# Kernel tuning notes

Measured on AMD Instinct MI355X. Metric: run time of the kernel, lower is better.

## Reference

```python
import jax, jax.numpy as jnp
import numpy as np

GRID = 12  # sqrt(144), seq_len = 144 fixed by w_g shape


def _relative_position(n: int) -> jnp.ndarray:
    # grid cell centers for an n x n grid, flattened row-major -> (n*n,)
    idx = np.arange(n * n)
    row, col = idx // n, idx % n
    cx = (col + 0.5) / n  # (x_min + x_max)/2 with x_min=col/n, x_max=(col+1)/n
    cy = (row + 0.5) / n
    dx = cx[:, None] - cx[None, :]
    dy = cy[:, None] - cy[None, :]
    ax = np.sign(dx) * 0.5
    ay = np.sign(dy) * 0.5
    dx = np.abs(np.log(np.abs(dx) + 0.5))
    dy = np.abs(np.log(np.abs(dy) + 0.5))
    # cat along leading dim then permute(1,2,0) == stack last-dim in order (dx,dy,ax,ay)
    pos = np.stack([dx, dy, ax, ay], axis=-1).astype(np.float32)  # (S,S,4)
    return jnp.asarray(pos)


def setup_inputs() -> dict:
    key = jax.random.key(0)
    ks = jax.random.split(key, 9)
    B, S, D = 128, GRID * GRID, 1024
    sc = 1.0 / np.sqrt(D)
    return {
        "query": jax.random.normal(ks[0], (B, S, D), jnp.float32),
        "key": jax.random.normal(ks[1], (B, S, D), jnp.float32),
        "value": jax.random.normal(ks[2], (B, S, D), jnp.float32),
        "Wq": jax.random.normal(ks[3], (D, D), jnp.float32) * sc,
        "bq": jnp.zeros((D,), jnp.float32),
        "Wk": jax.random.normal(ks[4], (D, D), jnp.float32) * sc,
        "bk": jnp.zeros((D,), jnp.float32),
        "Wv": jax.random.normal(ks[5], (D, D), jnp.float32) * sc,
        "bv": jnp.zeros((D,), jnp.float32),
        "Wlin": jax.random.normal(ks[6], (D, 4), jnp.float32) * 0.5,
        "w_g": jax.random.normal(ks[7], (S, D, 1), jnp.float32) * sc,
    }


def reference(query, key, value, Wq, bq, Wk, bk, Wv, bv, Wlin, w_g):
    d_model = query.shape[-1]
    # QKV projections + ReLU activation (dropout is identity at eval)
    q = jax.nn.relu(jnp.einsum("bsd,ed->bse", query, Wq) + bq)
    k = jax.nn.relu(jnp.einsum("bsd,ed->bse", key, Wk) + bk)
    v = jax.nn.relu(jnp.einsum("bsd,ed->bse", value, Wv) + bv)
    # raw scores: (B, S, S)
    att = jnp.einsum("bsd,btd->bst", q, k) * (d_model ** -0.5)
    # relative-position bias: (S, S, 4) -> linear -> relu -> per-row w_g -> relu
    pos = _relative_position(GRID)
    rp = jax.nn.relu(jnp.einsum("stf,df->std", pos, Wlin))  # (S, S, D)
    rp = jax.nn.relu(jnp.einsum("std,sdo->sto", rp, w_g)[..., 0])  # (S, S)
    att = jax.nn.softmax(att + rp[None, :, :], axis=-1)
    return jnp.einsum("bst,btd->bsd", att, v)
```

## Files before the change

### kernel.cpp

```cpp
#include <hip/hip_runtime.h>
#include <hip/hip_fp16.h>

#define DEV __device__ __forceinline__

using half8 = __attribute__((ext_vector_type(8))) _Float16;
using half4 = __attribute__((ext_vector_type(4))) _Float16;
using f32x4 = __attribute__((ext_vector_type(4))) float;

DEV void gload_lds16(const void* g, void* l) {
  __builtin_amdgcn_global_load_lds((const __attribute__((address_space(1))) unsigned int*)g,
                                   (__attribute__((address_space(3))) unsigned int*)l,
                                   16, 0, 0);
}

DEV f32x4 mfma16x32(half8 a, half8 b, f32x4 c) {
  return __builtin_amdgcn_mfma_f32_16x16x32_f16(a, b, c, 0, 0, 0);
}

__global__ void conv3_f32_f16(const float* __restrict__ s0, const float* __restrict__ s1,
                              const float* __restrict__ s2, _Float16* __restrict__ d0,
                              _Float16* __restrict__ d1, _Float16* __restrict__ d2, int n) {
  const float* s = blockIdx.z == 0 ? s0 : (blockIdx.z == 1 ? s1 : s2);
  _Float16* d = blockIdx.z == 0 ? d0 : (blockIdx.z == 1 ? d1 : d2);
  int i = (blockIdx.x * 256 + threadIdx.x) * 8;
  if (i >= n) return;
  float4 a = *(const float4*)(s + i);
  float4 b = *(const float4*)(s + i + 4);
  half8 h;
  h[0] = (_Float16)a.x; h[1] = (_Float16)a.y; h[2] = (_Float16)a.z; h[3] = (_Float16)a.w;
  h[4] = (_Float16)b.x; h[5] = (_Float16)b.y; h[6] = (_Float16)b.z; h[7] = (_Float16)b.w;
  *(half8*)(d + i) = h;
}

__global__ __launch_bounds__(192) void rp_kernel(const float* __restrict__ Wlin,
                                                 const float* __restrict__ wg,
                                                 float* __restrict__ rp) {
  int s = blockIdx.x, t = threadIdx.x;
  if (t >= 144) return;
  int rs = s / 12, cs = s % 12, rt = t / 12, ct = t % 12;
  float dx = (cs - ct) / 12.f, dy = (rs - rt) / 12.f;
  float ax = (dx > 0.f) ? 0.5f : (dx < 0.f ? -0.5f : 0.f);
  float ay = (dy > 0.f) ? 0.5f : (dy < 0.f ? -0.5f : 0.f);
  float lx = fabsf(logf(fabsf(dx) + 0.5f));
  float ly = fabsf(logf(fabsf(dy) + 0.5f));
  float a0 = 0.f, a1 = 0.f, a2 = 0.f, a3 = 0.f;
  const float* wgs = wg + s * 1024;
  for (int d = 0; d < 1024; d += 4) {
#pragma unroll
    for (int u = 0; u < 4; ++u) {
      float4 w = *(const float4*)(Wlin + (d + u) * 4);
      float dot = lx * w.x + ly * w.y + ax * w.z + ay * w.w;
      dot = dot > 0.f ? dot : 0.f;
      float p = dot * wgs[d + u];
      if (u == 0) a0 += p; else if (u == 1) a1 += p; else if (u == 2) a2 += p; else a3 += p;
    }
  }
  float acc = (a0 + a1) + (a2 + a3);
  rp[s * 144 + t] = acc > 0.f ? acc : 0.f;
}

__global__ __launch_bounds__(256, 2) void gemm_proj(
    const _Float16* __restrict__ a0q, const _Float16* __restrict__ a1q,
    const _Float16* __restrict__ a2q, const _Float16* __restrict__ w0q,
    const _Float16* __restrict__ w1q, const _Float16* __restrict__ w2q,
    const float* __restrict__ bi0, const float* __restrict__ bi1,
    const float* __restrict__ bi2, _Float16* __restrict__ c0q,
    _Float16* __restrict__ c1q, _Float16* __restrict__ c2q) {
  const _Float16* A = blockIdx.z == 0 ? a0q : (blockIdx.z == 1 ? a1q : a2q);
  const _Float16* W = blockIdx.z == 0 ? w0q : (blockIdx.z == 1 ? w1q : w2q);
  const float* bias = blockIdx.z == 0 ? bi0 : (blockIdx.z == 1 ? bi1 : bi2);
  _Float16* C = blockIdx.z == 0 ? c0q : (blockIdx.z == 1 ? c1q : c2q);

  __shared__ __align__(16) char lds[73728];
  int tid = threadIdx.x, wid = tid >> 6, lane = tid & 63;
  int lin = blockIdx.y * 8 + blockIdx.x;
  int local = lin >> 3;
  int mt = (lin & 7) * 9 + (local >> 3), nt = local & 7;
  int m0 = mt * 256, n0 = nt * 128;

  int r4l = lane >> 2, c4 = lane & 3;
  int cg8 = ((c4 + (r4l >> 1)) & 3) * 8;
  int lr = lane & 15, lg = lane >> 4;
  int rdoff = lr * 64 + ((lg - (lr >> 1)) & 3) * 16;

  const _Float16* gp[6];
#pragma unroll
  for (int c = 0; c < 6; ++c) {
    int q = c * 4 + wid;
    gp[c] = (q < 16) ? A + (size_t)(m0 + q * 16 + r4l) * 1024 + cg8
                     : W + (size_t)(n0 + (q - 16) * 16 + r4l) * 1024 + cg8;
  }
  char *sl0 = lds, *sl1 = lds + 24576, *sl2 = lds + 49152;
  auto issue = [&](char* slot) {
#pragma unroll
    for (int c = 0; c < 6; ++c) { gload_lds16(gp[c], slot + (c * 4 + wid) * 1024); gp[c] += 32; }
  };
  issue(sl0);
  issue(sl1);
  f32x4 acc[8][4] = {};
  int abase = (wid >> 1) * 8192, bbase = 16384 + (wid & 1) * 4096;
  for (int t = 0; t < 32; ++t) {
    asm volatile("s_waitcnt vmcnt(6)" ::: "memory");
    __builtin_amdgcn_s_barrier();
    __builtin_amdgcn_sched_barrier(0);
    issue(sl2);
    half8 a[8], b[4];
#pragma unroll
    for (int i = 0; i < 8; ++i) a[i] = *(const half8*)(sl0 + abase + i * 1024 + rdoff);
#pragma unroll
    for (int j = 0; j < 4; ++j) b[j] = *(const half8*)(sl0 + bbase + j * 1024 + rdoff);
#pragma unroll
    for (int i = 0; i < 8; ++i)
#pragma unroll
      for (int j = 0; j < 4; ++j)
        acc[i][j] = mfma16x32(b[j], a[i], acc[i][j]);
    char* tmp = sl0; sl0 = sl1; sl1 = sl2; sl2 = tmp;
  }
  int wm = (wid >> 1) * 128, wn = (wid & 1) * 64;
#pragma unroll
  for (int i = 0; i < 8; ++i) {
    int row = m0 + wm + i * 16 + lr;
#pragma unroll
    for (int j = 0; j < 4; ++j) {
      int col = n0 + wn + j * 16 + lg * 4;
      float4 b4 = *(const float4*)(bias + col);
      half4 h;
      float v0 = acc[i][j][0] + b4.x; h[0] = (_Float16)(v0 > 0.f ? v0 : 0.f);
      float v1 = acc[i][j][1] + b4.y; h[1] = (_Float16)(v1 > 0.f ? v1 : 0.f);
      float v2 = acc[i][j][2] + b4.z; h[2] = (_Float16)(v2 > 0.f ? v2 : 0.f);
      float v3 = acc[i][j][3] + b4.w; h[3] = (_Float16)(v3 > 0.f ? v3 : 0.f);
      *(half4*)(C + (size_t)row * 1024 + col) = h;
    }
  }
}

__global__ __launch_bounds__(256) void transpose_v(const _Float16* __restrict__ v,
                                                   _Float16* __restrict__ vt) {
  __shared__ _Float16 t[64][65];
  int b = blockIdx.z, e0 = blockIdx.x * 64, s0 = blockIdx.y * 64;
  int c = threadIdx.x & 63, r4 = threadIdx.x >> 6;
#pragma unroll
  for (int p = 0; p < 16; ++p) {
    int r = p * 4 + r4;
    t[r][c] = (s0 + r < 144) ? v[(size_t)(b * 144 + s0 + r) * 1024 + e0 + c] : (_Float16)0.f;
  }
  __syncthreads();
#pragma unroll
  for (int p = 0; p < 16; ++p) {
    int i = p * 4 + r4;
    if (s0 + c < 160) vt[(size_t)(b * 1024 + e0 + i) * 160 + s0 + c] = t[c][i];
  }
}

__global__ __launch_bounds__(256) void attn_kernel(const _Float16* __restrict__ q,
                                                   const _Float16* __restrict__ k,
                                                   const _Float16* __restrict__ vt,
                                                   const float* __restrict__ rp,
                                                   float* __restrict__ out) {
  __shared__ __align__(16) char lds[53248];
  float* sc = (float*)lds;
  _Float16* P = (_Float16*)(lds + 36864);
  float* sums = (float*)(lds + 52992);

  int tid = threadIdx.x, wid = tid >> 6, lane = tid & 63;
  int lin = blockIdx.y * 3 + blockIdx.x;
  int swz = (lin & 7) * 48 + (lin >> 3);
  int mt3 = swz % 3, b = swz / 3;
  int m0 = mt3 * 48;
  const int nstart_t[4] = {0, 3, 5, 7};
  const int ncnt_t[4]   = {3, 2, 2, 2};
  int ns = nstart_t[wid], nc = ncnt_t[wid];
  int r4l = lane >> 2, c4 = lane & 3;
  int cg8 = ((c4 + (r4l >> 1)) & 3) * 8;
  int lr = lane & 15, lg = lane >> 4;
  int rdoff = lr * 64 + ((lg - (lr >> 1)) & 3) * 16;

  {
    char *sl0 = lds, *sl1 = lds + 12288, *sl2 = lds + 24576;
    const _Float16* g1[3];
#pragma unroll
    for (int c = 0; c < 3; ++c) {
      int qq = c * 4 + wid;
      g1[c] = (qq < 3) ? q + (size_t)(b * 144 + m0 + qq * 16 + r4l) * 1024 + cg8
                       : k + (size_t)(b * 144 + (qq - 3) * 16 + r4l) * 1024 + cg8;
    }
    auto issue1 = [&](char* slot) {
#pragma unroll
      for (int c = 0; c < 3; ++c) {
        gload_lds16(g1[c], slot + (c * 4 + wid) * 1024);
        g1[c] += 32;
      }
    };
    issue1(sl0);
    issue1(sl1);
    f32x4 acc[3][3] = {};
    for (int t = 0; t < 32; ++t) {
      asm volatile("s_waitcnt vmcnt(3)" ::: "memory");
      __builtin_amdgcn_sched_barrier(0);
      __builtin_amdgcn_s_barrier();
      __builtin_amdgcn_sched_barrier(0);
      issue1(sl2);
      half8 af[3], bf[3];
#pragma unroll
      for (int i = 0; i < 3; ++i)
        af[i] = *(const half8*)(sl0 + i * 1024 + rdoff);
#pragma unroll
      for (int j = 0; j < 3; ++j)
        if (j < nc)
          bf[j] = *(const half8*)(sl0 + (3 + ns + j) * 1024 + rdoff);
#pragma unroll
      for (int i = 0; i < 3; ++i)
#pragma unroll
        for (int j = 0; j < 3; ++j)
          if (j < nc)
            acc[i][j] = mfma16x32(bf[j], af[i], acc[i][j]);
      char* tmp = sl0; sl0 = sl1; sl1 = sl2; sl2 = tmp;
    }
    asm volatile("s_waitcnt vmcnt(0)" ::: "memory");
    __syncthreads();
    const float scale = 0.03125f;
#pragma unroll
    for (int i = 0; i < 3; ++i) {
      int qrow = i * 16 + lr;
#pragma unroll
      for (int j = 0; j < 3; ++j)
        if (j < nc) {
          int kc0 = (ns + j) * 16 + lg * 4;
          float4 rr = *(const float4*)(rp + (m0 + qrow) * 144 + kc0);
          f32x4 vs;
          vs[0] = acc[i][j][0] * scale + rr.x;
          vs[1] = acc[i][j][1] * scale + rr.y;
          vs[2] = acc[i][j][2] * scale + rr.z;
          vs[3] = acc[i][j][3] * scale + rr.w;
          *(f32x4*)(sc + qrow * 152 + kc0) = vs;
        }
    }
  }
  __syncthreads();

  if (tid < 192) {
    int r = tid >> 2, qd = tid & 3;
    int cb = qd * 36;
    float m = -1e30f;
    for (int c2 = 0; c2 < 36; ++c2) m = fmaxf(m, sc[r * 152 + cb + c2]);
    m = fmaxf(m, __shfl_xor(m, 1));
    m = fmaxf(m, __shfl_xor(m, 2));
    float s = 0.f;
    for (int c2 = 0; c2 < 36; ++c2) {
      float e = __expf(sc[r * 152 + cb + c2] - m);
      s += e;
      P[r * 168 + cb + c2] = (_Float16)e;
    }
    s += __shfl_xor(s, 1);
    s += __shfl_xor(s, 2);
    if (qd == 0) sums[r] = s;
  }
  if (tid < 96) {
    int r = tid >> 1, c0 = 144 + (tid & 1) * 8;
    *(half8*)(P + r * 168 + c0) = (half8){};
  }
  __syncthreads();

  char *s0p = lds, *s1p = lds + 16384;
  auto issue2 = [&](int idx, char* slot) {
    int nn0 = (idx / 5) * 256, kk0 = (idx % 5) * 32;
#pragma unroll
    for (int c = 0; c < 4; ++c) {
      int ch = c * 4 + wid;
      gload_lds16(vt + (size_t)(b * 1024 + nn0 + ch * 16 + r4l) * 160 + kk0 + cg8,
                  slot + ch * 1024);
    }
  };
  issue2(0, s0p);
  f32x4 o[3][4] = {};
  for (int it = 0; it < 20; ++it) {
    asm volatile("s_waitcnt vmcnt(0)" ::: "memory");
    __builtin_amdgcn_sched_barrier(0);
    __builtin_amdgcn_s_barrier();
    __builtin_amdgcn_sched_barrier(0);
    issue2(it + 1, ((it + 1) & 1) ? s1p : s0p);
    char* sb = (it & 1) ? s1p : s0p;
    int k0 = (it % 5) * 32;
    half8 af[3], bf[4];
#pragma unroll
    for (int i = 0; i < 3; ++i)
      af[i] = *(const half8*)(P + (i * 16 + lr) * 168 + k0 + lg * 8);
#pragma unroll
    for (int j = 0; j < 4; ++j)
      bf[j] = *(const half8*)(sb + (wid * 4 + j) * 1024 + rdoff);
#pragma unroll
    for (int i = 0; i < 3; ++i)
#pragma unroll
      for (int j = 0; j < 4; ++j)
        o[i][j] = mfma16x32(bf[j], af[i], o[i][j]);
    if (it % 5 == 4) {
      int n0 = (it / 5) * 256;
#pragma unroll
      for (int i = 0; i < 3; ++i) {
        int row = i * 16 + lr;
        float inv = 1.f / sums[row];
#pragma unroll
        for (int j = 0; j < 4; ++j) {
          f32x4 vo;
          vo[0] = o[i][j][0] * inv; vo[1] = o[i][j][1] * inv;
          vo[2] = o[i][j][2] * inv; vo[3] = o[i][j][3] * inv;
          *(f32x4*)(out + (size_t)(b * 144 + m0 + row) * 1024 + n0 + wid * 64 + j * 16 + lg * 4) = vo;
          o[i][j] = (f32x4){};
        }
      }
    }
  }
}

extern "C" void kernel_launch(void* const* d_in, const int* in_sizes, int n_in,
                              void* d_out, int out_size, void* d_ws, size_t ws_size,
                              hipStream_t stream) {
  const float* query = (const float*)d_in[0];
  const float* key   = (const float*)d_in[1];
  const float* value = (const float*)d_in[2];
  const float* Wq    = (const float*)d_in[3];
  const float* bq    = (const float*)d_in[4];
  const float* Wk    = (const float*)d_in[5];
  const float* bk    = (const float*)d_in[6];
  const float* Wv    = (const float*)d_in[7];
  const float* bv    = (const float*)d_in[8];
  const float* Wlin  = (const float*)d_in[9];
  const float* wg    = (const float*)d_in[10];
  float* out = (float*)d_out;

  char* ws = (char*)d_ws;
  const size_t NQKV = (size_t)18432 * 1024;
  const size_t NVT  = (size_t)131072 * 160;
  const int    NW   = 1024 * 1024;
  _Float16* Wqb = (_Float16*)(ws);
  _Float16* Wkb = (_Float16*)(ws + (2u << 20));
  _Float16* Wvb = (_Float16*)(ws + (4u << 20));
  _Float16* qp  = (_Float16*)(ws + (6u << 20));
  _Float16* kp  = qp + NQKV;
  _Float16* vp  = kp + NQKV;

  dim3 tgrid(16, 3, 128), agrid(3, 128);

  if (ws_size >= 238000000ull) {
    _Float16* ia = vp + NQKV;
    _Float16* ib = ia + NQKV;
    _Float16* ic = ib + NQKV;
    _Float16* vt = ic;
    float*    rp = (float*)((char*)(ic + NVT) + 65536);
    conv3_f32_f16<<<dim3((int)(NQKV / 2048), 1, 3), 256, 0, stream>>>(
        query, key, value, ia, ib, ic, (int)NQKV);
    conv3_f32_f16<<<dim3(NW / 2048, 1, 3), 256, 0, stream>>>(Wq, Wk, Wv, Wqb, Wkb, Wvb, NW);
    rp_kernel<<<144, 192, 0, stream>>>(Wlin, wg, rp);
    gemm_proj<<<dim3(8, 72, 3), 256, 0, stream>>>(ia, ib, ic, Wqb, Wkb, Wvb,
                                                  bq, bk, bv, qp, kp, vp);
    transpose_v<<<tgrid, 256, 0, stream>>>(vp, vt);
    attn_kernel<<<agrid, 256, 0, stream>>>(qp, kp, vt, rp, out);
  } else {
    _Float16* inb = vp + NQKV;
    _Float16* vt  = inb;
    float*    rp  = (float*)(inb + NVT + 65536);
    rp_kernel<<<144, 192, 0, stream>>>(Wlin, wg, rp);
    conv3_f32_f16<<<dim3(NW / 2048, 1, 3), 256, 0, stream>>>(Wq, Wk, Wv, Wqb, Wkb, Wvb, NW);
    conv3_f32_f16<<<dim3((int)(NQKV / 2048), 1, 1), 256, 0, stream>>>(
        query, query, query, inb, inb, inb, (int)NQKV);
    gemm_proj<<<dim3(8, 72, 1), 256, 0, stream>>>(inb, inb, inb, Wqb, Wqb, Wqb,
                                                  bq, bq, bq, qp, qp, qp);
    conv3_f32_f16<<<dim3((int)(NQKV / 2048), 1, 1), 256, 0, stream>>>(
        key, key, key, inb, inb, inb, (int)NQKV);
    gemm_proj<<<dim3(8, 72, 1), 256, 0, stream>>>(inb, inb, inb, Wkb, Wkb, Wkb,
                                                  bk, bk, bk, kp, kp, kp);
    conv3_f32_f16<<<dim3((int)(NQKV / 2048), 1, 1), 256, 0, stream>>>(
        value, value, value, inb, inb, inb, (int)NQKV);
    gemm_proj<<<dim3(8, 72, 1), 256, 0, stream>>>(inb, inb, inb, Wvb, Wvb, Wvb,
                                                  bv, bv, bv, vp, vp, vp);
    transpose_v<<<tgrid, 256, 0, stream>>>(vp, vt);
    attn_kernel<<<agrid, 256, 0, stream>>>(qp, kp, vt, rp, out);
  }
}
```

Measured before the change: 331.7 us.

## Restructure projection GEMM to 256x256 tiles with 8 waves and phased ping-pong pipeline

The QKV projection GEMM moves from 256-thread blocks with 256x128 tiles to 512-thread blocks with 256x256 tiles and 128KB LDS. The K loop is split into half-k phases over a double-buffered LDS layout, with fine-grained async loads issued between MFMA groups and s_setprio raised around the MFMA bursts. The goal is more data reuse per load and better overlap of global-to-LDS transfers with matrix math. In exchange it uses more LDS and registers per block, which may cut occupancy, and adds many barriers.

```diff
diff --git a/kernel.cpp b/kernel.cpp
--- a/kernel.cpp
+++ b/kernel.cpp
@@ -59,7 +59,7 @@
   rp[s * 144 + t] = acc > 0.f ? acc : 0.f;
 }
 
-__global__ __launch_bounds__(256, 2) void gemm_proj(
+__global__ __launch_bounds__(512, 2) void gemm_proj(
     const _Float16* __restrict__ a0q, const _Float16* __restrict__ a1q,
     const _Float16* __restrict__ a2q, const _Float16* __restrict__ w0q,
     const _Float16* __restrict__ w1q, const _Float16* __restrict__ w2q,
@@ -71,58 +71,109 @@
   const float* bias = blockIdx.z == 0 ? bi0 : (blockIdx.z == 1 ? bi1 : bi2);
   _Float16* C = blockIdx.z == 0 ? c0q : (blockIdx.z == 1 ? c1q : c2q);
 
-  __shared__ __align__(16) char lds[73728];
+  __shared__ __align__(16) char lds[131072];
   int tid = threadIdx.x, wid = tid >> 6, lane = tid & 63;
-  int lin = blockIdx.y * 8 + blockIdx.x;
+  int lin = blockIdx.y * 4 + blockIdx.x;
   int local = lin >> 3;
-  int mt = (lin & 7) * 9 + (local >> 3), nt = local & 7;
-  int m0 = mt * 256, n0 = nt * 128;
+  int mt = (lin & 7) * 9 + (local >> 2), nt = local & 3;
+  int m0 = mt * 256, n0 = nt * 256;
+  int wm = wid >> 2, wn = wid & 3;
 
   int r4l = lane >> 2, c4 = lane & 3;
   int cg8 = ((c4 + (r4l >> 1)) & 3) * 8;
   int lr = lane & 15, lg = lane >> 4;
   int rdoff = lr * 64 + ((lg - (lr >> 1)) & 3) * 16;
 
-  const _Float16* gp[6];
-#pragma unroll
-  for (int c = 0; c < 6; ++c) {
-    int q = c * 4 + wid;
-    gp[c] = (q < 16) ? A + (size_t)(m0 + q * 16 + r4l) * 1024 + cg8
-                     : W + (size_t)(n0 + (q - 16) * 16 + r4l) * 1024 + cg8;
-  }
-  char *sl0 = lds, *sl1 = lds + 24576, *sl2 = lds + 49152;
-  auto issue = [&](char* slot) {
-#pragma unroll
-    for (int c = 0; c < 6; ++c) { gload_lds16(gp[c], slot + (c * 4 + wid) * 1024); gp[c] += 32; }
-  };
-  issue(sl0);
-  issue(sl1);
+  const _Float16* pA = A + (size_t)(m0 + wid * 16 + r4l) * 1024 + cg8;
+  const _Float16* pB = W + (size_t)(n0 + wid * 16 + r4l) * 1024 + cg8;
+
+#define ISSUE(KT, KH, HF) do {                                                   \
+    int ktc_ = (KT) < 16 ? (KT) : 15;                                            \
+    int koff_ = ktc_ * 64 + (KH) * 32;                                           \
+    char* sb_ = lds + (((KT) & 1) << 16) + ((KH) << 14);                         \
+    gload_lds16(pA + (size_t)(HF) * 131072 + koff_,                              \
+                sb_ + (wid + (HF) * 8) * 1024);                                  \
+    gload_lds16(pB + (size_t)(HF) * 131072 + koff_,                              \
+                sb_ + 32768 + (wid + (HF) * 8) * 1024);                          \
+  } while (0)
+
+#define PHASE(PAR, KH, MH, SKT, SKH, SH) do {                                    \
+    const char* qb_ = lds + ((PAR) << 16) + ((KH) << 14);                        \
+    half8 a0_ = *(const half8*)(qb_ + (wm * 8 + (MH) * 4 + 0) * 1024 + rdoff);   \
+    half8 a1_ = *(const half8*)(qb_ + (wm * 8 + (MH) * 4 + 1) * 1024 + rdoff);   \
+    half8 a2_ = *(const half8*)(qb_ + (wm * 8 + (MH) * 4 + 2) * 1024 + rdoff);   \
+    half8 a3_ = *(const half8*)(qb_ + (wm * 8 + (MH) * 4 + 3) * 1024 + rdoff);   \
+    if ((MH) == 0) {                                                             \
+      b0 = *(const half8*)(qb_ + 32768 + (wn * 4 + 0) * 1024 + rdoff);           \
+      b1 = *(const half8*)(qb_ + 32768 + (wn * 4 + 1) * 1024 + rdoff);           \
+      b2 = *(const half8*)(qb_ + 32768 + (wn * 4 + 2) * 1024 + rdoff);           \
+      b3 = *(const half8*)(qb_ + 32768 + (wn * 4 + 3) * 1024 + rdoff);           \
+    }                                                                            \
+    ISSUE(SKT, SKH, SH);                                                         \
+    __builtin_amdgcn_sched_barrier(0);                                           \
+    __builtin_amdgcn_s_barrier();                                                \
+    __builtin_amdgcn_sched_barrier(0);                                           \
+    __builtin_amdgcn_s_setprio(1);                                               \
+    acc[(MH)*4+0][0] = mfma16x32(b0, a0_, acc[(MH)*4+0][0]);                     \
+    acc[(MH)*4+0][1] = mfma16x32(b1, a0_, acc[(MH)*4+0][1]);                     \
+    acc[(MH)*4+0][2] = mfma16x32(b2, a0_, acc[(MH)*4+0][2]);                     \
+    acc[(MH)*4+0][3] = mfma16x32(b3, a0_, acc[(MH)*4+0][3]);                     \
+    acc[(MH)*4+1][0] = mfma16x32(b0, a1_, acc[(MH)*4+1][0]);                     \
+    acc[(MH)*4+1][1] = mfma16x32(b1, a1_, acc[(MH)*4+1][1]);                     \
+    acc[(MH)*4+1][2] = mfma16x32(b2, a1_, acc[(MH)*4+1][2]);                     \
+    acc[(MH)*4+1][3] = mfma16x32(b3, a1_, acc[(MH)*4+1][3]);                     \
+    acc[(MH)*4+2][0] = mfma16x32(b0, a2_, acc[(MH)*4+2][0]);                     \
+    acc[(MH)*4+2][1] = mfma16x32(b1, a2_, acc[(MH)*4+2][1]);                     \
+    acc[(MH)*4+2][2] = mfma16x32(b2, a2_, acc[(MH)*4+2][2]);                     \
+    acc[(MH)*4+2][3] = mfma16x32(b3, a2_, acc[(MH)*4+2][3]);                     \
+    acc[(MH)*4+3][0] = mfma16x32(b0, a3_, acc[(MH)*4+3][0]);                     \
+    acc[(MH)*4+3][1] = mfma16x32(b1, a3_, acc[(MH)*4+3][1]);                     \
+    acc[(MH)*4+3][2] = mfma16x32(b2, a3_, acc[(MH)*4+3][2]);                     \
+    acc[(MH)*4+3][3] = mfma16x32(b3, a3_, acc[(MH)*4+3][3]);                     \
+    __builtin_amdgcn_s_setprio(0);                                               \
+  } while (0)
+
+  ISSUE(0, 0, 0); ISSUE(0, 0, 1);
+  ISSUE(0, 1, 0); ISSUE(0, 1, 1);
+  ISSUE(1, 0, 0); ISSUE(1, 0, 1);
   f32x4 acc[8][4] = {};
-  int abase = (wid >> 1) * 8192, bbase = 16384 + (wid & 1) * 4096;
-  for (int t = 0; t < 32; ++t) {
-    asm volatile("s_waitcnt vmcnt(6)" ::: "memory");
-    __builtin_amdgcn_s_barrier();
+  half8 b0, b1, b2, b3;
+  asm volatile("s_waitcnt vmcnt(4)" ::: "memory");
+  __builtin_amdgcn_sched_barrier(0);
+  __builtin_amdgcn_s_barrier();
+
+  for (int m = 0; m < 8; ++m) {
+    int t0 = 2 * m;
+    PHASE(0, 0, 0, t0 + 1, 1, 0);
+    __builtin_amdgcn_s_barrier();
+    PHASE(0, 0, 1, t0 + 1, 1, 1);
+    __builtin_amdgcn_s_barrier();
+    PHASE(0, 1, 0, t0 + 2, 0, 0);
+    __builtin_amdgcn_s_barrier();
+    PHASE(0, 1, 1, t0 + 2, 0, 1);
+    asm volatile("s_waitcnt vmcnt(4)" ::: "memory");
     __builtin_amdgcn_sched_barrier(0);
-    issue(sl2);
-    half8 a[8], b[4];
-#pragma unroll
-    for (int i = 0; i < 8; ++i) a[i] = *(const half8*)(sl0 + abase + i * 1024 + rdoff);
-#pragma unroll
-    for (int j = 0; j < 4; ++j) b[j] = *(const half8*)(sl0 + bbase + j * 1024 + rdoff);
-#pragma unroll
-    for (int i = 0; i < 8; ++i)
-#pragma unroll
-      for (int j = 0; j < 4; ++j)
-        acc[i][j] = mfma16x32(b[j], a[i], acc[i][j]);
-    char* tmp = sl0; sl0 = sl1; sl1 = sl2; sl2 = tmp;
-  }
-  int wm = (wid >> 1) * 128, wn = (wid & 1) * 64;
+    __builtin_amdgcn_s_barrier();
+    PHASE(1, 0, 0, t0 + 2, 1, 0);
+    __builtin_amdgcn_s_barrier();
+    PHASE(1, 0, 1, t0 + 2, 1, 1);
+    __builtin_amdgcn_s_barrier();
+    PHASE(1, 1, 0, t0 + 3, 0, 0);
+    __builtin_amdgcn_s_barrier();
+    PHASE(1, 1, 1, t0 + 3, 0, 1);
+    asm volatile("s_waitcnt vmcnt(4)" ::: "memory");
+    __builtin_amdgcn_sched_barrier(0);
+    __builtin_amdgcn_s_barrier();
+  }
+#undef PHASE
+#undef ISSUE
+
 #pragma unroll
   for (int i = 0; i < 8; ++i) {
-    int row = m0 + wm + i * 16 + lr;
+    int row = m0 + wm * 128 + i * 16 + lr;
 #pragma unroll
     for (int j = 0; j < 4; ++j) {
-      int col = n0 + wn + j * 16 + lg * 4;
+      int col = n0 + wn * 64 + j * 16 + lg * 4;
       float4 b4 = *(const float4*)(bias + col);
       half4 h;
       float v0 = acc[i][j][0] + b4.x; h[0] = (_Float16)(v0 > 0.f ? v0 : 0.f);
@@ -351,7 +402,7 @@
         query, key, value, ia, ib, ic, (int)NQKV);
     conv3_f32_f16<<<dim3(NW / 2048, 1, 3), 256, 0, stream>>>(Wq, Wk, Wv, Wqb, Wkb, Wvb, NW);
     rp_kernel<<<144, 192, 0, stream>>>(Wlin, wg, rp);
-    gemm_proj<<<dim3(8, 72, 3), 256, 0, stream>>>(ia, ib, ic, Wqb, Wkb, Wvb,
+    gemm_proj<<<dim3(4, 72, 3), 512, 0, stream>>>(ia, ib, ic, Wqb, Wkb, Wvb,
                                                   bq, bk, bv, qp, kp, vp);
     transpose_v<<<tgrid, 256, 0, stream>>>(vp, vt);
     attn_kernel<<<agrid, 256, 0, stream>>>(qp, kp, vt, rp, out);
@@ -363,15 +414,15 @@
     conv3_f32_f16<<<dim3(NW / 2048, 1, 3), 256, 0, stream>>>(Wq, Wk, Wv, Wqb, Wkb, Wvb, NW);
     conv3_f32_f16<<<dim3((int)(NQKV / 2048), 1, 1), 256, 0, stream>>>(
         query, query, query, inb, inb, inb, (int)NQKV);
-    gemm_proj<<<dim3(8, 72, 1), 256, 0, stream>>>(inb, inb, inb, Wqb, Wqb, Wqb,
+    gemm_proj<<<dim3(4, 72, 1), 512, 0, stream>>>(inb, inb, inb, Wqb, Wqb, Wqb,
                                                   bq, bq, bq, qp, qp, qp);
     conv3_f32_f16<<<dim3((int)(NQKV / 2048), 1, 1), 256, 0, stream>>>(
         key, key, key, inb, inb, inb, (int)NQKV);
-    gemm_proj<<<dim3(8, 72, 1), 256, 0, stream>>>(inb, inb, inb, Wkb, Wkb, Wkb,
+    gemm_proj<<<dim3(4, 72, 1), 512, 0, stream>>>(inb, inb, inb, Wkb, Wkb, Wkb,
                                                   bk, bk, bk, kp, kp, kp);
     conv3_f32_f16<<<dim3((int)(NQKV / 2048), 1, 1), 256, 0, stream>>>(
         value, value, value, inb, inb, inb, (int)NQKV);
-    gemm_proj<<<dim3(8, 72, 1), 256, 0, stream>>>(inb, inb, inb, Wvb, Wvb, Wvb,
+    gemm_proj<<<dim3(4, 72, 1), 512, 0, stream>>>(inb, inb, inb, Wvb, Wvb, Wvb,
                                                   bv, bv, bv, vp, vp, vp);
     transpose_v<<<tgrid, 256, 0, stream>>>(vp, vt);
     attn_kernel<<<agrid, 256, 0, stream>>>(qp, kp, vt, rp, out);
```

Result: slower. 343.7 us (+3.6%).

## Fuse fp32-to-fp16 activation conversion into projection GEMM A-tile loading

Applied to the files above, without the earlier changes.

The projection GEMM now reads fp32 activations directly into registers, converts them to fp16 and writes them to LDS itself, with register double-buffering two steps ahead, while the weight tile still uses direct global-to-LDS loads. This removes the separate conversion pass over the three 18M-element inputs and its write and re-read of fp16 copies, and collapses the two workspace-size paths into one. The cost is twice the global bytes per A tile inside the GEMM, extra VGPR pressure, and conversion ALU work competing with MFMA issue under the 2-block occupancy bound.

```diff
diff --git a/kernel.cpp b/kernel.cpp
--- a/kernel.cpp
+++ b/kernel.cpp
@@ -60,13 +60,13 @@
 }
 
 __global__ __launch_bounds__(256, 2) void gemm_proj(
-    const _Float16* __restrict__ a0q, const _Float16* __restrict__ a1q,
-    const _Float16* __restrict__ a2q, const _Float16* __restrict__ w0q,
+    const float* __restrict__ A0, const float* __restrict__ A1,
+    const float* __restrict__ A2, const _Float16* __restrict__ w0q,
     const _Float16* __restrict__ w1q, const _Float16* __restrict__ w2q,
     const float* __restrict__ bi0, const float* __restrict__ bi1,
     const float* __restrict__ bi2, _Float16* __restrict__ c0q,
     _Float16* __restrict__ c1q, _Float16* __restrict__ c2q) {
-  const _Float16* A = blockIdx.z == 0 ? a0q : (blockIdx.z == 1 ? a1q : a2q);
+  const float* A = blockIdx.z == 0 ? A0 : (blockIdx.z == 1 ? A1 : A2);
   const _Float16* W = blockIdx.z == 0 ? w0q : (blockIdx.z == 1 ? w1q : w2q);
   const float* bias = blockIdx.z == 0 ? bi0 : (blockIdx.z == 1 ? bi1 : bi2);
   _Float16* C = blockIdx.z == 0 ? c0q : (blockIdx.z == 1 ? c1q : c2q);
@@ -83,39 +83,77 @@
   int lr = lane & 15, lg = lane >> 4;
   int rdoff = lr * 64 + ((lg - (lr >> 1)) & 3) * 16;
 
-  const _Float16* gp[6];
-#pragma unroll
-  for (int c = 0; c < 6; ++c) {
-    int q = c * 4 + wid;
-    gp[c] = (q < 16) ? A + (size_t)(m0 + q * 16 + r4l) * 1024 + cg8
-                     : W + (size_t)(n0 + (q - 16) * 16 + r4l) * 1024 + cg8;
-  }
+  const float* pA[4];
+#pragma unroll
+  for (int c = 0; c < 4; ++c)
+    pA[c] = A + (size_t)(m0 + (c * 4 + wid) * 16 + r4l) * 1024 + cg8;
+  const _Float16* pB[2];
+#pragma unroll
+  for (int c = 0; c < 2; ++c)
+    pB[c] = W + (size_t)(n0 + (c * 4 + wid) * 16 + r4l) * 1024 + cg8;
+
   char *sl0 = lds, *sl1 = lds + 24576, *sl2 = lds + 49152;
-  auto issue = [&](char* slot) {
-#pragma unroll
-    for (int c = 0; c < 6; ++c) { gload_lds16(gp[c], slot + (c * 4 + wid) * 1024); gp[c] += 32; }
-  };
-  issue(sl0);
-  issue(sl1);
+
+#define LOADA(RG, TT) do { int kk_ = ((TT) < 32 ? (TT) : 31) * 32;             \
+    _Pragma("unroll") for (int c = 0; c < 4; ++c) {                            \
+      RG[c * 2]     = *(const float4*)(pA[c] + kk_);                           \
+      RG[c * 2 + 1] = *(const float4*)(pA[c] + kk_ + 4);                       \
+    } } while (0)
+
+#define ISSUEB(TT, SLOT) do { int kk_ = ((TT) < 32 ? (TT) : 31) * 32;          \
+    _Pragma("unroll") for (int c = 0; c < 2; ++c)                              \
+      gload_lds16(pB[c] + kk_, (SLOT) + (16 + c * 4 + wid) * 1024);            \
+    } while (0)
+
+#define DSWRITE(RG, SLOT) do {                                                 \
+    _Pragma("unroll") for (int c = 0; c < 4; ++c) {                            \
+      half8 h_;                                                                \
+      h_[0] = (_Float16)RG[c * 2].x;     h_[1] = (_Float16)RG[c * 2].y;        \
+      h_[2] = (_Float16)RG[c * 2].z;     h_[3] = (_Float16)RG[c * 2].w;        \
+      h_[4] = (_Float16)RG[c * 2 + 1].x; h_[5] = (_Float16)RG[c * 2 + 1].y;    \
+      h_[6] = (_Float16)RG[c * 2 + 1].z; h_[7] = (_Float16)RG[c * 2 + 1].w;    \
+      *(half8*)((SLOT) + (c * 4 + wid) * 1024 + lane * 16) = h_;               \
+    } } while (0)
+
+  float4 rA[8], rB[8];
+  LOADA(rA, 0);
+  ISSUEB(0, sl0);
+  asm volatile("s_waitcnt vmcnt(0)" ::: "memory");
+  DSWRITE(rA, sl0);
+  LOADA(rB, 1);
+  ISSUEB(1, sl1);
   f32x4 acc[8][4] = {};
   int abase = (wid >> 1) * 8192, bbase = 16384 + (wid & 1) * 4096;
-  for (int t = 0; t < 32; ++t) {
-    asm volatile("s_waitcnt vmcnt(6)" ::: "memory");
-    __builtin_amdgcn_s_barrier();
-    __builtin_amdgcn_sched_barrier(0);
-    issue(sl2);
-    half8 a[8], b[4];
-#pragma unroll
-    for (int i = 0; i < 8; ++i) a[i] = *(const half8*)(sl0 + abase + i * 1024 + rdoff);
-#pragma unroll
-    for (int j = 0; j < 4; ++j) b[j] = *(const half8*)(sl0 + bbase + j * 1024 + rdoff);
-#pragma unroll
-    for (int i = 0; i < 8; ++i)
-#pragma unroll
-      for (int j = 0; j < 4; ++j)
-        acc[i][j] = mfma16x32(b[j], a[i], acc[i][j]);
-    char* tmp = sl0; sl0 = sl1; sl1 = sl2; sl2 = tmp;
-  }
+
+#define GBODY(REGC, REGN, T) do {                                              \
+    LOADA(REGN, (T) + 2);                                                      \
+    asm volatile("s_waitcnt vmcnt(10)" ::: "memory");                          \
+    asm volatile("s_waitcnt lgkmcnt(0)" ::: "memory");                         \
+    __builtin_amdgcn_sched_barrier(0);                                         \
+    __builtin_amdgcn_s_barrier();                                              \
+    __builtin_amdgcn_sched_barrier(0);                                         \
+    ISSUEB((T) + 2, sl2);                                                      \
+    half8 a_[8], b_[4];                                                        \
+    _Pragma("unroll") for (int i = 0; i < 8; ++i)                              \
+      a_[i] = *(const half8*)(sl0 + abase + i * 1024 + rdoff);                 \
+    _Pragma("unroll") for (int j = 0; j < 4; ++j)                              \
+      b_[j] = *(const half8*)(sl0 + bbase + j * 1024 + rdoff);                 \
+    DSWRITE(REGC, sl1);                                                        \
+    _Pragma("unroll") for (int i = 0; i < 8; ++i)                              \
+      _Pragma("unroll") for (int j = 0; j < 4; ++j)                            \
+        acc[i][j] = mfma16x32(b_[j], a_[i], acc[i][j]);           \
+    char* tmp_ = sl0; sl0 = sl1; sl1 = sl2; sl2 = tmp_;                        \
+  } while (0)
+
+  for (int tp = 0; tp < 16; ++tp) {
+    GBODY(rB, rA, 2 * tp);
+    GBODY(rA, rB, 2 * tp + 1);
+  }
+#undef GBODY
+#undef DSWRITE
+#undef ISSUEB
+#undef LOADA
+
   int wm = (wid >> 1) * 128, wn = (wid & 1) * 64;
 #pragma unroll
   for (int i = 0; i < 8; ++i) {
@@ -338,42 +376,15 @@
   _Float16* qp  = (_Float16*)(ws + (6u << 20));
   _Float16* kp  = qp + NQKV;
   _Float16* vp  = kp + NQKV;
+  _Float16* vt  = vp + NQKV;
+  float*    rp  = (float*)((char*)(vt + NVT) + 65536);
 
   dim3 tgrid(16, 3, 128), agrid(3, 128);
 
-  if (ws_size >= 238000000ull) {
-    _Float16* ia = vp + NQKV;
-    _Float16* ib = ia + NQKV;
-    _Float16* ic = ib + NQKV;
-    _Float16* vt = ic;
-    float*    rp = (float*)((char*)(ic + NVT) + 65536);
-    conv3_f32_f16<<<dim3((int)(NQKV / 2048), 1, 3), 256, 0, stream>>>(
-        query, key, value, ia, ib, ic, (int)NQKV);
-    conv3_f32_f16<<<dim3(NW / 2048, 1, 3), 256, 0, stream>>>(Wq, Wk, Wv, Wqb, Wkb, Wvb, NW);
-    rp_kernel<<<144, 192, 0, stream>>>(Wlin, wg, rp);
-    gemm_proj<<<dim3(8, 72, 3), 256, 0, stream>>>(ia, ib, ic, Wqb, Wkb, Wvb,
-                                                  bq, bk, bv, qp, kp, vp);
-    transpose_v<<<tgrid, 256, 0, stream>>>(vp, vt);
-    attn_kernel<<<agrid, 256, 0, stream>>>(qp, kp, vt, rp, out);
-  } else {
-    _Float16* inb = vp + NQKV;
-    _Float16* vt  = inb;
-    float*    rp  = (float*)(inb + NVT + 65536);
-    rp_kernel<<<144, 192, 0, stream>>>(Wlin, wg, rp);
-    conv3_f32_f16<<<dim3(NW / 2048, 1, 3), 256, 0, stream>>>(Wq, Wk, Wv, Wqb, Wkb, Wvb, NW);
-    conv3_f32_f16<<<dim3((int)(NQKV / 2048), 1, 1), 256, 0, stream>>>(
-        query, query, query, inb, inb, inb, (int)NQKV);
-    gemm_proj<<<dim3(8, 72, 1), 256, 0, stream>>>(inb, inb, inb, Wqb, Wqb, Wqb,
-                                                  bq, bq, bq, qp, qp, qp);
-    conv3_f32_f16<<<dim3((int)(NQKV / 2048), 1, 1), 256, 0, stream>>>(
-        key, key, key, inb, inb, inb, (int)NQKV);
-    gemm_proj<<<dim3(8, 72, 1), 256, 0, stream>>>(inb, inb, inb, Wkb, Wkb, Wkb,
-                                                  bk, bk, bk, kp, kp, kp);
-    conv3_f32_f16<<<dim3((int)(NQKV / 2048), 1, 1), 256, 0, stream>>>(
-        value, value, value, inb, inb, inb, (int)NQKV);
-    gemm_proj<<<dim3(8, 72, 1), 256, 0, stream>>>(inb, inb, inb, Wvb, Wvb, Wvb,
-                                                  bv, bv, bv, vp, vp, vp);
-    transpose_v<<<tgrid, 256, 0, stream>>>(vp, vt);
-    attn_kernel<<<agrid, 256, 0, stream>>>(qp, kp, vt, rp, out);
-  }
-}
+  conv3_f32_f16<<<dim3(NW / 2048, 1, 3), 256, 0, stream>>>(Wq, Wk, Wv, Wqb, Wkb, Wvb, NW);
+  rp_kernel<<<144, 192, 0, stream>>>(Wlin, wg, rp);
+  gemm_proj<<<dim3(8, 72, 3), 256, 0, stream>>>(query, key, value, Wqb, Wkb, Wvb,
+                                                bq, bk, bv, qp, kp, vp);
+  transpose_v<<<tgrid, 256, 0, stream>>>(vp, vt);
+  attn_kernel<<<agrid, 256, 0, stream>>>(qp, kp, vt, rp, out);
+}
```

Result: slower. 359.4 us (+8.3%).

## Fuse V transpose into projection GEMM epilogue and drop transpose kernel

Applied to the files above, without the earlier changes.

The V projection GEMM now writes its output directly in the transposed, 160-padded layout the attention kernel reads, which removes the separate transpose_v kernel and the full round trip of the V intermediate through memory. A small kernel zeroes the padding columns (144..159) of each transposed row up front. The cost is that the fused epilogue does scattered 2-byte stores strided by 160 elements instead of coalesced half4 stores, which may hurt write efficiency. The workspace layout is reorganised to make room for the rp buffer and the new vt location.

```diff
diff --git a/kernel.cpp b/kernel.cpp
--- a/kernel.cpp
+++ b/kernel.cpp
@@ -30,6 +30,13 @@
   h[0] = (_Float16)a.x; h[1] = (_Float16)a.y; h[2] = (_Float16)a.z; h[3] = (_Float16)a.w;
   h[4] = (_Float16)b.x; h[5] = (_Float16)b.y; h[6] = (_Float16)b.z; h[7] = (_Float16)b.w;
   *(half8*)(d + i) = h;
+}
+
+__global__ void vt_pad_zero(_Float16* __restrict__ vt) {
+  int i = blockIdx.x * 256 + threadIdx.x;
+  _Float16* p = vt + (size_t)i * 160 + 144;
+  *(half8*)p = (half8){};
+  *(half8*)(p + 8) = (half8){};
 }
 
 __global__ __launch_bounds__(192) void rp_kernel(const float* __restrict__ Wlin,
@@ -65,7 +72,8 @@
     const _Float16* __restrict__ w1q, const _Float16* __restrict__ w2q,
     const float* __restrict__ bi0, const float* __restrict__ bi1,
     const float* __restrict__ bi2, _Float16* __restrict__ c0q,
-    _Float16* __restrict__ c1q, _Float16* __restrict__ c2q) {
+    _Float16* __restrict__ c1q, _Float16* __restrict__ c2q,
+    _Float16* __restrict__ vtp, int vtz) {
   const _Float16* A = blockIdx.z == 0 ? a0q : (blockIdx.z == 1 ? a1q : a2q);
   const _Float16* W = blockIdx.z == 0 ? w0q : (blockIdx.z == 1 ? w1q : w2q);
   const float* bias = blockIdx.z == 0 ? bi0 : (blockIdx.z == 1 ? bi1 : bi2);
@@ -117,6 +125,7 @@
     char* tmp = sl0; sl0 = sl1; sl1 = sl2; sl2 = tmp;
   }
   int wm = (wid >> 1) * 128, wn = (wid & 1) * 64;
+  bool tov = (vtp != nullptr) && ((int)blockIdx.z == vtz);
 #pragma unroll
   for (int i = 0; i < 8; ++i) {
     int row = m0 + wm + i * 16 + lr;
@@ -129,26 +138,14 @@
       float v1 = acc[i][j][1] + b4.y; h[1] = (_Float16)(v1 > 0.f ? v1 : 0.f);
       float v2 = acc[i][j][2] + b4.z; h[2] = (_Float16)(v2 > 0.f ? v2 : 0.f);
       float v3 = acc[i][j][3] + b4.w; h[3] = (_Float16)(v3 > 0.f ? v3 : 0.f);
-      *(half4*)(C + (size_t)row * 1024 + col) = h;
-    }
-  }
-}
-
-__global__ __launch_bounds__(256) void transpose_v(const _Float16* __restrict__ v,
-                                                   _Float16* __restrict__ vt) {
-  __shared__ _Float16 t[64][65];
-  int b = blockIdx.z, e0 = blockIdx.x * 64, s0 = blockIdx.y * 64;
-  int c = threadIdx.x & 63, r4 = threadIdx.x >> 6;
-#pragma unroll
-  for (int p = 0; p < 16; ++p) {
-    int r = p * 4 + r4;
-    t[r][c] = (s0 + r < 144) ? v[(size_t)(b * 144 + s0 + r) * 1024 + e0 + c] : (_Float16)0.f;
-  }
-  __syncthreads();
-#pragma unroll
-  for (int p = 0; p < 16; ++p) {
-    int i = p * 4 + r4;
-    if (s0 + c < 160) vt[(size_t)(b * 1024 + e0 + i) * 160 + s0 + c] = t[c][i];
+      if (tov) {
+        int bb = row / 144, ss = row - bb * 144;
+        _Float16* vb = vtp + (size_t)(bb * 1024 + col) * 160 + ss;
+        vb[0] = h[0]; vb[160] = h[1]; vb[320] = h[2]; vb[480] = h[3];
+      } else {
+        *(half4*)(C + (size_t)row * 1024 + col) = h;
+      }
+    }
   }
 }
 
@@ -335,45 +332,44 @@
   _Float16* Wqb = (_Float16*)(ws);
   _Float16* Wkb = (_Float16*)(ws + (2u << 20));
   _Float16* Wvb = (_Float16*)(ws + (4u << 20));
-  _Float16* qp  = (_Float16*)(ws + (6u << 20));
+  float*    rp  = (float*)(ws + (6u << 20));
+  _Float16* qp  = (_Float16*)(ws + (6u << 20) + 131072);
   _Float16* kp  = qp + NQKV;
-  _Float16* vp  = kp + NQKV;
-
-  dim3 tgrid(16, 3, 128), agrid(3, 128);
+  _Float16* vt  = kp + NQKV;
+
+  dim3 agrid(3, 128);
 
   if (ws_size >= 238000000ull) {
-    _Float16* ia = vp + NQKV;
+    _Float16* ia = vt + NVT + 32768;
     _Float16* ib = ia + NQKV;
     _Float16* ic = ib + NQKV;
-    _Float16* vt = ic;
-    float*    rp = (float*)((char*)(ic + NVT) + 65536);
     conv3_f32_f16<<<dim3((int)(NQKV / 2048), 1, 3), 256, 0, stream>>>(
         query, key, value, ia, ib, ic, (int)NQKV);
     conv3_f32_f16<<<dim3(NW / 2048, 1, 3), 256, 0, stream>>>(Wq, Wk, Wv, Wqb, Wkb, Wvb, NW);
     rp_kernel<<<144, 192, 0, stream>>>(Wlin, wg, rp);
+    vt_pad_zero<<<512, 256, 0, stream>>>(vt);
     gemm_proj<<<dim3(8, 72, 3), 256, 0, stream>>>(ia, ib, ic, Wqb, Wkb, Wvb,
-                                                  bq, bk, bv, qp, kp, vp);
-    transpose_v<<<tgrid, 256, 0, stream>>>(vp, vt);
+                                                  bq, bk, bv, qp, kp, kp ,
+                                                  vt, 2);
     attn_kernel<<<agrid, 256, 0, stream>>>(qp, kp, vt, rp, out);
   } else {
-    _Float16* inb = vp + NQKV;
-    _Float16* vt  = inb;
-    float*    rp  = (float*)(inb + NVT + 65536);
+    _Float16* inb = vt + NVT;
     rp_kernel<<<144, 192, 0, stream>>>(Wlin, wg, rp);
+    vt_pad_zero<<<512, 256, 0, stream>>>(vt);
     conv3_f32_f16<<<dim3(NW / 2048, 1, 3), 256, 0, stream>>>(Wq, Wk, Wv, Wqb, Wkb, Wvb, NW);
     conv3_f32_f16<<<dim3((int)(NQKV / 2048), 1, 1), 256, 0, stream>>>(
         query, query, query, inb, inb, inb, (int)NQKV);
     gemm_proj<<<dim3(8, 72, 1), 256, 0, stream>>>(inb, inb, inb, Wqb, Wqb, Wqb,
-                                                  bq, bq, bq, qp, qp, qp);
+                                                  bq, bq, bq, qp, qp, qp, nullptr, -1);
     conv3_f32_f16<<<dim3((int)(NQKV / 2048), 1, 1), 256, 0, stream>>>(
         key, key, key, inb, inb, inb, (int)NQKV);
     gemm_proj<<<dim3(8, 72, 1), 256, 0, stream>>>(inb, inb, inb, Wkb, Wkb, Wkb,
-                                                  bk, bk, bk, kp, kp, kp);
+                                                  bk, bk, bk, kp, kp, kp, nullptr, -1);
     conv3_f32_f16<<<dim3((int)(NQKV / 2048), 1, 1), 256, 0, stream>>>(
         value, value, value, inb, inb, inb, (int)NQKV);
     gemm_proj<<<dim3(8, 72, 1), 256, 0, stream>>>(inb, inb, inb, Wvb, Wvb, Wvb,
-                                                  bv, bv, bv, vp, vp, vp);
-    transpose_v<<<tgrid, 256, 0, stream>>>(vp, vt);
+                                                  bv, bv, bv, qp , qp, qp,
+                                                  vt, 0);
     attn_kernel<<<agrid, 256, 0, stream>>>(qp, kp, vt, rp, out);
   }
 }
```

Result: faster. 319.3 us (-3.7%).
